# Kernel optimization log

Hardware: AMD Instinct MI355X
Metric: run time of the kernel (lower is better)

The kernel has to match this reference:

```python
import jax, jax.numpy as jnp
import numpy as np

N = 320      # points per coordinate axis
RANK = 64    # CP rank = features[-1]
H = 128      # hidden width
DIMS = 3     # input_dim


def setup_inputs() -> dict:
    key = jax.random.key(0)
    ks = jax.random.split(key, 6)
    s0 = (6.0 / (1 + H)) ** 0.5   # xavier-uniform-ish scale for 1->H
    s1 = (6.0 / (H + H)) ** 0.5
    s2 = (6.0 / (H + RANK)) ** 0.5
    return {
        "xs": jax.random.normal(ks[0], (DIMS, N, 1), dtype=jnp.float32),
        "W0": jax.random.uniform(ks[1], (DIMS, 1, H), jnp.float32, -s0, s0),
        "b0": jnp.zeros((DIMS, H), jnp.float32),
        "W1": jax.random.uniform(ks[2], (DIMS, H, H), jnp.float32, -s1, s1),
        "b1": jnp.zeros((DIMS, H), jnp.float32),
        "W2": jax.random.uniform(ks[3], (DIMS, H, H), jnp.float32, -s1, s1),
        "b2": jnp.zeros((DIMS, H), jnp.float32),
        "W3": jax.random.uniform(ks[4], (DIMS, H, RANK), jnp.float32, -s2, s2),
        "b3": jnp.zeros((DIMS, RANK), jnp.float32),
    }


def reference(xs, W0, b0, W1, b1, W2, b2, W3, b3):
    # Per-coordinate MLP (identical to independent Dense stacks in the flax loop),
    # vmapped over the DIMS leading axis of stacked params.
    def mlp(x, w0, bb0, w1, bb1, w2, bb2, w3, bb3):
        h = jnp.tanh(x @ w0 + bb0)          # (N, H)
        h = jnp.tanh(h @ w1 + bb1)          # (N, H)
        h = jnp.tanh(h @ w2 + bb2)          # (N, H)
        return h @ w3 + bb3                 # (N, R)

    outs = jax.vmap(mlp)(xs, W0, b0, W1, b1, W2, b2, W3, b3)  # (DIMS, N, R)
    f = jnp.transpose(outs, (0, 2, 1))                         # (DIMS, R, N)
    # CP reconstruction: 'ra,rb,rc->abc' over shared rank r
    return jnp.einsum('ra,rb,rc->abc', f[0], f[1], f[2])
```

## Files before the change

kernel.cpp:

```cpp
#include <hip/hip_runtime.h>
#include <math.h>

#define DIMS 3
#define NPTS 320
#define HID  128
#define RANK 64
#define CH   160
#define LROW 128

typedef __attribute__((ext_vector_type(8)))  short bf16x8;
typedef __attribute__((ext_vector_type(16))) float f32x16;

static __device__ __forceinline__ unsigned short f2bf_rn(float x) {
    union { float f; unsigned int u; } v; v.f = x;
    unsigned int r = v.u + 0x7fffu + ((v.u >> 16) & 1u);
    return (unsigned short)(r >> 16);
}
static __device__ __forceinline__ float bf2f(unsigned short h) {
    union { unsigned int u; float f; } v; v.u = ((unsigned int)h) << 16;
    return v.f;
}

__global__ __launch_bounds__(512)
void mlp_kernel(const float* __restrict__ xs,
                const float* __restrict__ W0, const float* __restrict__ b0,
                const float* __restrict__ W1, const float* __restrict__ b1,
                const float* __restrict__ W2, const float* __restrict__ b2,
                const float* __restrict__ W3, const float* __restrict__ b3,
                float* __restrict__ f01t,
                unsigned short* __restrict__ f2hi) {
    const int blk = blockIdx.x;
    const int d = blk / NPTS, n = blk % NPTS;
    const int j  = threadIdx.x & (HID - 1);
    const int kq = threadIdx.x >> 7;
    const int k0 = kq * 32;

    __shared__ float ha[HID];
    __shared__ float hb[HID];
    __shared__ float part[4][HID];

    const float x = xs[d * NPTS + n];

    if (kq == 0) {
        ha[j] = tanhf(fmaf(x, W0[d * HID + j], b0[d * HID + j]));
    }
    __syncthreads();

    {
        float acc = 0.0f;
        const float* w = W1 + d * HID * HID + j;
        #pragma unroll 16
        for (int k = 0; k < 32; ++k) acc = fmaf(ha[k0 + k], w[(k0 + k) * HID], acc);
        part[kq][j] = acc;
    }
    __syncthreads();
    if (kq == 0) {
        float s = ((part[0][j] + part[1][j]) + (part[2][j] + part[3][j]))
                  + b1[d * HID + j];
        hb[j] = tanhf(s);
    }
    __syncthreads();

    {
        float acc = 0.0f;
        const float* w = W2 + d * HID * HID + j;
        #pragma unroll 16
        for (int k = 0; k < 32; ++k) acc = fmaf(hb[k0 + k], w[(k0 + k) * HID], acc);
        part[kq][j] = acc;
    }
    __syncthreads();
    if (kq == 0) {
        float s = ((part[0][j] + part[1][j]) + (part[2][j] + part[3][j]))
                  + b2[d * HID + j];
        ha[j] = tanhf(s);
    }
    __syncthreads();

    if (j < RANK) {
        float acc = 0.0f;
        const float* w = W3 + d * HID * RANK + j;
        #pragma unroll 16
        for (int k = 0; k < 32; ++k) acc = fmaf(ha[k0 + k], w[(k0 + k) * RANK], acc);
        part[kq][j] = acc;
    }
    __syncthreads();
    if (kq == 0 && j < RANK) {
        float s = ((part[0][j] + part[1][j]) + (part[2][j] + part[3][j]))
                  + b3[d * RANK + j];
        if (d == 0) {
            f01t[n * RANK + j] = s;
        } else if (d == 1) {
            f01t[(NPTS + n) * RANK + j] = s;
        } else {
            f2hi[n * RANK + j] = f2bf_rn(s);
        }
    }
}

__global__ __launch_bounds__(128, 4)
void cp_mfma_kernel(const float* __restrict__ f01t,
                    const unsigned short* __restrict__ f2hi,
                    float* __restrict__ out) {
    const int tx = threadIdx.x;
    const int w  = tx >> 6;
    const int l  = tx & 63;
    const int lc = l & 31;
    const int hw = l >> 5;

    const int c0 = (blockIdx.x & 1) * CH;

    __shared__ char sB[CH * LROW];

    #pragma unroll
    for (int i = 0; i < 10; ++i) {
        int idx = tx + i * 128;
        int row = idx >> 3;
        int g   = (idx & 7) << 4;
        *(float4*)(&sB[row * LROW + (g ^ ((row & 7) << 4))]) =
            ((const float4*)f2hi)[c0 * 8 + idx];
    }
    __syncthreads();

    for (int t = blockIdx.x >> 1; t < NPTS * 5; t += 1024) {
        const int a   = t / 5;
        const int b0w = (t - a * 5) * 64 + w * 32;
        const float* f0p = f01t + (size_t)a * RANK + hw * 8;
        const float* f1p = f01t + (size_t)(NPTS + b0w + lc) * RANK + hw * 8;

        bf16x8 ahi[4], alo[4];
        #pragma unroll
        for (int ks = 0; ks < 4; ++ks) {
            const int k0 = ks * 16;
            float4 f0a = *(const float4*)(f0p + k0);
            float4 f0b = *(const float4*)(f0p + k0 + 4);
            float4 f1a = *(const float4*)(f1p + k0);
            float4 f1b = *(const float4*)(f1p + k0 + 4);

            float g[8];
            g[0] = f1a.x * f0a.x; g[1] = f1a.y * f0a.y;
            g[2] = f1a.z * f0a.z; g[3] = f1a.w * f0a.w;
            g[4] = f1b.x * f0b.x; g[5] = f1b.y * f0b.y;
            g[6] = f1b.z * f0b.z; g[7] = f1b.w * f0b.w;

            #pragma unroll
            for (int j = 0; j < 8; ++j) {
                unsigned short hi = f2bf_rn(g[j]);
                ahi[ks][j] = (short)hi;
                alo[ks][j] = (short)f2bf_rn(g[j] - bf2f(hi));
            }
        }

        #pragma unroll
        for (int ct = 0; ct < 5; ++ct) {
            const char* rowp = &sB[(ct * 32 + lc) * LROW];
            const int swz = ((ct * 32 + lc) & 7) << 4;

            f32x16 acc;
            #pragma unroll
            for (int jj = 0; jj < 16; ++jj) acc[jj] = 0.0f;

            #pragma unroll
            for (int ks = 0; ks < 4; ++ks) {
                const int base = ks * 32 + (hw << 4);
                bf16x8 b = *(const bf16x8*)(rowp + (base ^ swz));
                acc = __builtin_amdgcn_mfma_f32_32x32x16_bf16(ahi[ks], b, acc, 0, 0, 0);
                acc = __builtin_amdgcn_mfma_f32_32x32x16_bf16(alo[ks], b, acc, 0, 0, 0);
            }

            float* obase = out + ((size_t)a * NPTS + b0w) * NPTS + c0 + ct * 32 + lc;
            #pragma unroll
            for (int q = 0; q < 16; ++q) {
                int row = (q & 3) + 8 * (q >> 2) + 4 * hw;
                obase[(size_t)row * NPTS] = acc[q];
            }
        }
    }
}

extern "C" void kernel_launch(void* const* d_in, const int* in_sizes, int n_in,
                              void* d_out, int out_size, void* d_ws, size_t ws_size,
                              hipStream_t stream) {
    const float* xs = (const float*)d_in[0];
    const float* W0 = (const float*)d_in[1];
    const float* b0 = (const float*)d_in[2];
    const float* W1 = (const float*)d_in[3];
    const float* b1 = (const float*)d_in[4];
    const float* W2 = (const float*)d_in[5];
    const float* b2 = (const float*)d_in[6];
    const float* W3 = (const float*)d_in[7];
    const float* b3 = (const float*)d_in[8];

    float* f01t = (float*)d_ws;
    unsigned short* f2hi = (unsigned short*)((char*)d_ws + 2 * NPTS * RANK * 4);
    float* out = (float*)d_out;

    mlp_kernel<<<dim3(DIMS * NPTS), dim3(512), 0, stream>>>(
        xs, W0, b0, W1, b1, W2, b2, W3, b3, f01t, f2hi);

    cp_mfma_kernel<<<dim3(2048), dim3(128), 0, stream>>>(f01t, f2hi, out);
}
```

Baseline: 43.12 us.

## Persistent CP kernel with LDS-staged coalesced output and double-buffered tiles

The CP reconstruction kernel becomes a persistent kernel with 256 blocks. Each block holds the whole bf16 f2 factor in LDS and walks tiles of 32 b-rows by all 320 c-columns. MFMA results go into a double-buffered LDS staging area and are written out as contiguous float4 rows, while the f0/f1 operands for the next tile are prefetched. The aim is fully coalesced output stores and overlap of stores with compute, replacing the strided scattered writes. The cost is a large LDS footprint (~120KB), which allows only two waves per CU and may limit memory-level parallelism; strided LDS writes into the staging area may also cause bank conflicts.

```diff
diff --git a/kernel.cpp b/kernel.cpp
--- a/kernel.cpp
+++ b/kernel.cpp
@@ -5,8 +5,9 @@
 #define NPTS 320
 #define HID  128
 #define RANK 64
-#define CH   160
 #define LROW 128
+#define NT   3200
+#define GRID 256
 
 typedef __attribute__((ext_vector_type(8)))  short bf16x8;
 typedef __attribute__((ext_vector_type(16))) float f32x16;
@@ -97,7 +98,7 @@
     }
 }
 
-__global__ __launch_bounds__(128, 4)
+__global__ __launch_bounds__(128)
 void cp_mfma_kernel(const float* __restrict__ f01t,
                     const unsigned short* __restrict__ f2hi,
                     float* __restrict__ out) {
@@ -107,74 +108,124 @@
     const int lc = l & 31;
     const int hw = l >> 5;
 
-    const int c0 = (blockIdx.x & 1) * CH;
-
-    __shared__ char sB[CH * LROW];
+    __shared__ char  sB[NPTS * LROW];
+    __shared__ float stage[2][32 * NPTS];
 
     #pragma unroll
-    for (int i = 0; i < 10; ++i) {
+    for (int i = 0; i < 20; ++i) {
         int idx = tx + i * 128;
         int row = idx >> 3;
         int g   = (idx & 7) << 4;
         *(float4*)(&sB[row * LROW + (g ^ ((row & 7) << 4))]) =
-            ((const float4*)f2hi)[c0 * 8 + idx];
-    }
-    __syncthreads();
-
-    for (int t = blockIdx.x >> 1; t < NPTS * 5; t += 1024) {
-        const int a   = t / 5;
-        const int b0w = (t - a * 5) * 64 + w * 32;
-        const float* f0p = f01t + (size_t)a * RANK + hw * 8;
-        const float* f1p = f01t + (size_t)(NPTS + b0w + lc) * RANK + hw * 8;
-
-        bf16x8 ahi[4], alo[4];
-        #pragma unroll
-        for (int ks = 0; ks < 4; ++ks) {
-            const int k0 = ks * 16;
-            float4 f0a = *(const float4*)(f0p + k0);
-            float4 f0b = *(const float4*)(f0p + k0 + 4);
-            float4 f1a = *(const float4*)(f1p + k0);
-            float4 f1b = *(const float4*)(f1p + k0 + 4);
-
-            float g[8];
-            g[0] = f1a.x * f0a.x; g[1] = f1a.y * f0a.y;
-            g[2] = f1a.z * f0a.z; g[3] = f1a.w * f0a.w;
-            g[4] = f1b.x * f0b.x; g[5] = f1b.y * f0b.y;
-            g[6] = f1b.z * f0b.z; g[7] = f1b.w * f0b.w;
-
-            #pragma unroll
-            for (int j = 0; j < 8; ++j) {
-                unsigned short hi = f2bf_rn(g[j]);
-                ahi[ks][j] = (short)hi;
-                alo[ks][j] = (short)f2bf_rn(g[j] - bf2f(hi));
-            }
-        }
-
-        #pragma unroll
-        for (int ct = 0; ct < 5; ++ct) {
-            const char* rowp = &sB[(ct * 32 + lc) * LROW];
-            const int swz = ((ct * 32 + lc) & 7) << 4;
-
-            f32x16 acc;
-            #pragma unroll
-            for (int jj = 0; jj < 16; ++jj) acc[jj] = 0.0f;
-
-            #pragma unroll
-            for (int ks = 0; ks < 4; ++ks) {
-                const int base = ks * 32 + (hw << 4);
-                bf16x8 b = *(const bf16x8*)(rowp + (base ^ swz));
-                acc = __builtin_amdgcn_mfma_f32_32x32x16_bf16(ahi[ks], b, acc, 0, 0, 0);
-                acc = __builtin_amdgcn_mfma_f32_32x32x16_bf16(alo[ks], b, acc, 0, 0, 0);
-            }
-
-            float* obase = out + ((size_t)a * NPTS + b0w) * NPTS + c0 + ct * 32 + lc;
-            #pragma unroll
-            for (int q = 0; q < 16; ++q) {
-                int row = (q & 3) + 8 * (q >> 2) + 4 * hw;
-                obase[(size_t)row * NPTS] = acc[q];
-            }
-        }
-    }
+            ((const float4*)f2hi)[idx];
+    }
+    __syncthreads();
+
+    float4 L[4][4];
+    bf16x8 ahi[4], alo[4];
+
+#define ALOAD(T)                                                               \
+    {                                                                          \
+        const int a_  = (T) / 10;                                              \
+        const int b0_ = ((T) - a_ * 10) * 32;                                  \
+        const float* f0p = f01t + (size_t)a_ * RANK + hw * 8;                  \
+        const float* f1p = f01t + (size_t)(NPTS + b0_ + lc) * RANK + hw * 8;   \
+        _Pragma("unroll")                                                      \
+        for (int ks = 0; ks < 4; ++ks) {                                       \
+            L[ks][0] = *(const float4*)(f0p + ks * 16);                        \
+            L[ks][1] = *(const float4*)(f0p + ks * 16 + 4);                    \
+            L[ks][2] = *(const float4*)(f1p + ks * 16);                        \
+            L[ks][3] = *(const float4*)(f1p + ks * 16 + 4);                    \
+        }                                                                      \
+    }
+
+#define ABUILD()                                                               \
+    {                                                                          \
+        _Pragma("unroll")                                                      \
+        for (int ks = 0; ks < 4; ++ks) {                                       \
+            float4 f0a = L[ks][0], f0b = L[ks][1];                             \
+            float4 f1a = L[ks][2], f1b = L[ks][3];                             \
+            float g[8];                                                        \
+            g[0] = f1a.x * f0a.x; g[1] = f1a.y * f0a.y;                        \
+            g[2] = f1a.z * f0a.z; g[3] = f1a.w * f0a.w;                        \
+            g[4] = f1b.x * f0b.x; g[5] = f1b.y * f0b.y;                        \
+            g[6] = f1b.z * f0b.z; g[7] = f1b.w * f0b.w;                        \
+            _Pragma("unroll")                                                  \
+            for (int j = 0; j < 8; ++j) {                                      \
+                unsigned short hi = f2bf_rn(g[j]);                             \
+                ahi[ks][j] = (short)hi;                                        \
+                alo[ks][j] = (short)f2bf_rn(g[j] - bf2f(hi));                  \
+            }                                                                  \
+        }                                                                      \
+    }
+
+#define MFMA_STAGE(BUF)                                                        \
+    {                                                                          \
+        _Pragma("unroll")                                                      \
+        for (int ct = 0; ct < 5; ++ct) {                                       \
+            const int crow = w * 160 + ct * 32 + lc;                           \
+            const char* rowp = &sB[crow * LROW];                               \
+            const int swz = (crow & 7) << 4;                                   \
+            f32x16 acc;                                                        \
+            _Pragma("unroll")                                                  \
+            for (int jj = 0; jj < 16; ++jj) acc[jj] = 0.0f;                    \
+            _Pragma("unroll")                                                  \
+            for (int ks = 0; ks < 4; ++ks) {                                   \
+                const int base = ks * 32 + (hw << 4);                          \
+                bf16x8 b = *(const bf16x8*)(rowp + (base ^ swz));              \
+                acc = __builtin_amdgcn_mfma_f32_32x32x16_bf16(ahi[ks], b, acc, 0, 0, 0); \
+                acc = __builtin_amdgcn_mfma_f32_32x32x16_bf16(alo[ks], b, acc, 0, 0, 0); \
+            }                                                                  \
+            _Pragma("unroll")                                                  \
+            for (int q = 0; q < 16; ++q) {                                     \
+                int brow = (q & 3) + 8 * (q >> 2) + 4 * hw;                    \
+                stage[BUF][brow * NPTS + crow] = acc[q];                       \
+            }                                                                  \
+        }                                                                      \
+    }
+
+#define COPYOUT(T, BUF)                                                        \
+    {                                                                          \
+        const int a_  = (T) / 10;                                              \
+        const int b0_ = ((T) - a_ * 10) * 32;                                  \
+        float4* dst = (float4*)(out + ((size_t)a_ * NPTS + b0_) * NPTS);       \
+        const float4* src = (const float4*)stage[BUF];                         \
+        float4 tmp[20];                                                        \
+        _Pragma("unroll")                                                      \
+        for (int p = 0; p < 20; ++p) tmp[p] = src[tx + p * 128];               \
+        _Pragma("unroll")                                                      \
+        for (int p = 0; p < 20; ++p) dst[tx + p * 128] = tmp[p];               \
+    }
+
+    int t = blockIdx.x;
+    int cur = 0;
+
+    ALOAD(t)
+    ABUILD()
+    MFMA_STAGE(0)
+    asm volatile("s_waitcnt lgkmcnt(0)" ::: "memory");
+    __builtin_amdgcn_s_barrier();
+
+    for (;;) {
+        const int tn = t + GRID;
+        const bool more = (tn < NT);
+
+        if (more) ALOAD(tn)
+        __builtin_amdgcn_sched_barrier(0);
+        COPYOUT(t, cur)
+        if (!more) break;
+
+        ABUILD()
+        MFMA_STAGE(cur ^ 1)
+        asm volatile("s_waitcnt lgkmcnt(0)" ::: "memory");
+        __builtin_amdgcn_s_barrier();
+        t = tn; cur ^= 1;
+    }
+
+#undef ALOAD
+#undef ABUILD
+#undef MFMA_STAGE
+#undef COPYOUT
 }
 
 extern "C" void kernel_launch(void* const* d_in, const int* in_sizes, int n_in,
@@ -197,5 +248,5 @@
     mlp_kernel<<<dim3(DIMS * NPTS), dim3(512), 0, stream>>>(
         xs, W0, b0, W1, b1, W2, b2, W3, b3, f01t, f2hi);
 
-    cp_mfma_kernel<<<dim3(2048), dim3(128), 0, stream>>>(f01t, f2hi, out);
-}
+    cp_mfma_kernel<<<dim3(GRID), dim3(128), 0, stream>>>(f01t, f2hi, out);
+}
```

Result: slower. 49.29 us (+14.3%).
